# Kernel tuning notes

Hardware: AMD Instinct MI355X
Metric: run time of the kernel (lower is better)

Reference implementation:

```python
import jax, jax.numpy as jnp
import numpy as np

B, S, NQ, H, HD = 2, 4096, 576, 32, 128
HID = H * HD  # 4096


def setup_inputs() -> dict:
    key = jax.random.key(0)
    ks = jax.random.split(key, 7)
    sc = 0.02
    return {
        "hidden_states": jax.random.normal(ks[0], (B, S, HID), jnp.float32),
        "by_pass_hidden_states": jax.random.normal(ks[1], (B, NQ, HID), jnp.float32),
        "attention_mask": jnp.zeros((B, 1, S, NQ), jnp.float32),
        "Wq": jax.random.normal(ks[2], (HID, HID), jnp.float32) * sc,
        "Wk": jax.random.normal(ks[3], (HID, HID), jnp.float32) * sc,
        "Wv": jax.random.normal(ks[4], (HID, HID), jnp.float32) * sc,
        "Wo": jax.random.normal(ks[5], (HID, HID), jnp.float32) * sc,
    }


def reference(hidden_states, by_pass_hidden_states, attention_mask, Wq, Wk, Wv, Wo):
    b, s, _ = hidden_states.shape
    nq = by_pass_hidden_states.shape[1]
    # projections (nn.Linear applies x @ W.T); reshape to (b, heads, len, head_dim)
    q = (hidden_states @ Wq.T).reshape(b, s, H, HD).transpose(0, 2, 1, 3)
    k = (by_pass_hidden_states @ Wk.T).reshape(b, nq, H, HD).transpose(0, 2, 1, 3)
    v = (by_pass_hidden_states @ Wv.T).reshape(b, nq, H, HD).transpose(0, 2, 1, 3)
    # eager QK^T -> mask -> fp32 softmax -> V
    scores = jnp.einsum("bhsd,bhqd->bhsq", q, k) / jnp.sqrt(jnp.float32(HD))
    scores = scores + attention_mask  # (b,1,s,nq) broadcast over heads
    attn = jax.nn.softmax(scores.astype(jnp.float32), axis=-1).astype(q.dtype)
    out = jnp.einsum("bhsq,bhqd->bhsd", attn, v)
    out = out.transpose(0, 2, 1, 3).reshape(b, s, HID)
    return out @ Wo.T
```

## Files before the change

### kernel.cpp

```cpp
#include <hip/hip_runtime.h>
#include <stdint.h>

#define Bn   2
#define Sn   4096
#define NQn  576
#define Hn   32
#define HDn  128
#define HIDn 4096

typedef unsigned short bfu;
typedef short short8 __attribute__((ext_vector_type(8)));
typedef float f32x4 __attribute__((ext_vector_type(4)));

__device__ __forceinline__ bfu f2b(float f) {
  uint32_t x = __builtin_bit_cast(uint32_t, f);
  return (bfu)((x + 0x7fffu + ((x >> 16) & 1u)) >> 16);
}

__device__ __forceinline__ void gload16(const void* g, void* l) {
  __builtin_amdgcn_global_load_lds(
      (const __attribute__((address_space(1))) uint32_t*)g,
      (__attribute__((address_space(3))) uint32_t*)l, 16, 0, 0);
}

__global__ void cast_f32_bf16(const float* __restrict__ in, bfu* __restrict__ out,
                              int n8) {
  int i = blockIdx.x * 256 + threadIdx.x;
  if (i >= n8) return;
  const float4* in4 = (const float4*)in;
  float4 a = in4[2 * i], c = in4[2 * i + 1];
  short8 v;
  v[0] = (short)f2b(a.x); v[1] = (short)f2b(a.y);
  v[2] = (short)f2b(a.z); v[3] = (short)f2b(a.w);
  v[4] = (short)f2b(c.x); v[5] = (short)f2b(c.y);
  v[6] = (short)f2b(c.z); v[7] = (short)f2b(c.w);
  ((short8*)out)[i] = v;
}

template <int WRITE_BF16>
__global__ __launch_bounds__(512, 2)
void gemm_bt256(const bfu* __restrict__ A, const bfu* __restrict__ Bm,
                void* __restrict__ Cout, int M, int N, int K) {
  __shared__ __align__(16) bfu Asm[2][256 * 64];
  __shared__ __align__(16) bfu Bsm[2][256 * 64];
  const int tid = threadIdx.x;
  const int wave = tid >> 6, lane = tid & 63;
  const int lr = lane & 15, kq = lane >> 4;
  const int wm = wave >> 2, wn = wave & 3;
  const long m0 = (long)blockIdx.y * 256, n0 = (long)blockIdx.x * 256;
  const int NT = K >> 6;

  const int c0j = tid >> 3, c0c = tid & 7;
  const int c1j = (512 + tid) >> 3, c1c = tid & 7;
  const bfu* aSrc0 = A + (m0 + c0j) * (long)K + ((c0c ^ (c0j & 7)) * 8);
  const bfu* aSrc1 = A + (m0 + c1j) * (long)K + ((c1c ^ (c1j & 7)) * 8);
  const bfu* bSrc0 = Bm + (n0 + c0j) * (long)K + ((c0c ^ (c0j & 7)) * 8);
  const bfu* bSrc1 = Bm + (n0 + c1j) * (long)K + ((c1c ^ (c1j & 7)) * 8);

  auto stageA = [&](int t, int buf, int half) {
    long koff = (long)t * 64 + (long)half * 128 * K;
    gload16(aSrc0 + koff, &Asm[buf][half * 8192 + (wave * 64) * 8]);
    gload16(aSrc1 + koff, &Asm[buf][half * 8192 + (512 + wave * 64) * 8]);
  };
  auto stageB = [&](int t, int buf, int half) {
    long koff = (long)t * 64 + (long)half * 128 * K;
    gload16(bSrc0 + koff, &Bsm[buf][half * 8192 + (wave * 64) * 8]);
    gload16(bSrc1 + koff, &Bsm[buf][half * 8192 + (512 + wave * 64) * 8]);
  };
  auto ldsA = [&](int buf, int mf, int ks) -> short8 {
    int row = (mf >> 2) * 128 + wm * 64 + (mf & 3) * 16 + lr;
    int off = (row * 128 + ks * 64 + kq * 16) ^ ((row & 7) << 4);
    return *(const short8*)((const char*)Asm[buf] + off);
  };
  auto ldsB = [&](int buf, int nf, int ks) -> short8 {
    int row = (nf >> 1) * 128 + wn * 32 + (nf & 1) * 16 + lr;
    int off = (row * 128 + ks * 64 + kq * 16) ^ ((row & 7) << 4);
    return *(const short8*)((const char*)Bsm[buf] + off);
  };

  f32x4 acc[8][4] = {};

  stageA(0, 0, 0); stageB(0, 0, 0); stageB(0, 0, 1); stageA(0, 0, 1);
  asm volatile("s_waitcnt vmcnt(0)" ::: "memory");
  __builtin_amdgcn_s_barrier();

  for (int t = 0; t < NT; ++t) {
    const int buf = t & 1;
    if (t + 1 < NT) {
      stageA(t + 1, buf ^ 1, 0);
      stageB(t + 1, buf ^ 1, 0);
      stageB(t + 1, buf ^ 1, 1);
      stageA(t + 1, buf ^ 1, 1);
    }
    short8 a0[4][2], a1[4][2], b0[2][2], b1[2][2];
#pragma unroll
    for (int mf = 0; mf < 4; ++mf) {
      a0[mf][0] = ldsA(buf, mf, 0);
      a0[mf][1] = ldsA(buf, mf, 1);
    }
#pragma unroll
    for (int nf = 0; nf < 2; ++nf) {
      b0[nf][0] = ldsB(buf, nf, 0);
      b0[nf][1] = ldsB(buf, nf, 1);
      b1[nf][0] = ldsB(buf, 2 + nf, 0);
      b1[nf][1] = ldsB(buf, 2 + nf, 1);
    }
#pragma unroll
    for (int mf = 0; mf < 4; ++mf)
#pragma unroll
      for (int ks = 0; ks < 2; ++ks)
#pragma unroll
        for (int nf = 0; nf < 2; ++nf)
          acc[mf][nf] = __builtin_amdgcn_mfma_f32_16x16x32_bf16(
              a0[mf][ks], b0[nf][ks], acc[mf][nf], 0, 0, 0);
#pragma unroll
    for (int mf = 0; mf < 4; ++mf) {
      a1[mf][0] = ldsA(buf, 4 + mf, 0);
      a1[mf][1] = ldsA(buf, 4 + mf, 1);
    }
#pragma unroll
    for (int mf = 0; mf < 4; ++mf)
#pragma unroll
      for (int ks = 0; ks < 2; ++ks)
#pragma unroll
        for (int nf = 0; nf < 2; ++nf)
          acc[mf][2 + nf] = __builtin_amdgcn_mfma_f32_16x16x32_bf16(
              a0[mf][ks], b1[nf][ks], acc[mf][2 + nf], 0, 0, 0);
#pragma unroll
    for (int mf = 0; mf < 4; ++mf)
#pragma unroll
      for (int ks = 0; ks < 2; ++ks)
#pragma unroll
        for (int nf = 0; nf < 2; ++nf)
          acc[4 + mf][2 + nf] = __builtin_amdgcn_mfma_f32_16x16x32_bf16(
              a1[mf][ks], b1[nf][ks], acc[4 + mf][2 + nf], 0, 0, 0);
#pragma unroll
    for (int mf = 0; mf < 4; ++mf)
#pragma unroll
      for (int ks = 0; ks < 2; ++ks)
#pragma unroll
        for (int nf = 0; nf < 2; ++nf)
          acc[4 + mf][nf] = __builtin_amdgcn_mfma_f32_16x16x32_bf16(
              a1[mf][ks], b0[nf][ks], acc[4 + mf][nf], 0, 0, 0);
    asm volatile("s_waitcnt vmcnt(0)" ::: "memory");
    __builtin_amdgcn_s_barrier();
  }

#pragma unroll
  for (int mf = 0; mf < 8; ++mf)
#pragma unroll
    for (int nf = 0; nf < 4; ++nf)
#pragma unroll
      for (int r = 0; r < 4; ++r) {
        long row = m0 + (mf >> 2) * 128 + wm * 64 + (mf & 3) * 16 + kq * 4 + r;
        long col = n0 + (nf >> 1) * 128 + wn * 32 + (nf & 1) * 16 + lr;
        float v = acc[mf][nf][r];
        if (WRITE_BF16)
          ((bfu*)Cout)[row * N + col] = f2b(v);
        else
          ((float*)Cout)[row * N + col] = v;
      }
}

template <int WRITE_BF16>
__global__ __launch_bounds__(256, 2)
void gemm_bt(const bfu* __restrict__ A, const bfu* __restrict__ Bm,
             void* __restrict__ Cout, int M, int N, int K) {
  __shared__ __align__(16) bfu As[128 * 32];
  __shared__ __align__(16) bfu Bs[128 * 32];
  const int tid = threadIdx.x;
  const int wave = tid >> 6, lane = tid & 63;
  const int lr = lane & 15, kq = lane >> 4;
  const int wm = wave >> 1, wn = wave & 1;
  const long m0 = (long)blockIdx.y * 128, n0 = (long)blockIdx.x * 128;

  f32x4 acc[4][4] = {};

  for (int kk = 0; kk < K; kk += 32) {
#pragma unroll
    for (int i = 0; i < 2; ++i) {
      int tt = i * 256 + tid;
      long row = tt >> 2;
      int col = (tt & 3) * 8;
      gload16(A + (m0 + row) * K + kk + col, &As[(i * 256 + wave * 64) * 8]);
      gload16(Bm + (n0 + row) * K + kk + col, &Bs[(i * 256 + wave * 64) * 8]);
    }
    __syncthreads();
    short8 a[4], b[4];
#pragma unroll
    for (int mt = 0; mt < 4; ++mt)
      a[mt] = *(const short8*)&As[(wm * 64 + mt * 16 + lr) * 32 + kq * 8];
#pragma unroll
    for (int nt = 0; nt < 4; ++nt)
      b[nt] = *(const short8*)&Bs[(wn * 64 + nt * 16 + lr) * 32 + kq * 8];
#pragma unroll
    for (int mt = 0; mt < 4; ++mt)
#pragma unroll
      for (int nt = 0; nt < 4; ++nt)
        acc[mt][nt] = __builtin_amdgcn_mfma_f32_16x16x32_bf16(
            a[mt], b[nt], acc[mt][nt], 0, 0, 0);
    __syncthreads();
  }
#pragma unroll
  for (int mt = 0; mt < 4; ++mt)
#pragma unroll
    for (int nt = 0; nt < 4; ++nt)
#pragma unroll
      for (int r = 0; r < 4; ++r) {
        long row = m0 + wm * 64 + mt * 16 + kq * 4 + r;
        long col = n0 + wn * 64 + nt * 16 + lr;
        float v = acc[mt][nt][r];
        if (WRITE_BF16)
          ((bfu*)Cout)[row * N + col] = f2b(v);
        else
          ((float*)Cout)[row * N + col] = v;
      }
}

__global__ void transpose_v(const bfu* __restrict__ Vb, bfu* __restrict__ Vt) {
  __shared__ bfu t[32][33];
  const int bh = blockIdx.z;
  const int tq = blockIdx.x;
  const int td = blockIdx.y;
  const int b = bh >> 5, h = bh & 31;
  const int tx = threadIdx.x & 31, ty = threadIdx.x >> 5;
  const bfu* src = Vb + ((long)(b * NQn + tq * 32)) * HIDn + h * HDn + td * 32;
#pragma unroll
  for (int i = 0; i < 32; i += 8) t[ty + i][tx] = src[(long)(ty + i) * HIDn + tx];
  __syncthreads();
  bfu* dst = Vt + ((long)bh * HDn + td * 32) * NQn + tq * 32;
#pragma unroll
  for (int i = 0; i < 32; i += 8) dst[(long)(ty + i) * NQn + tx] = t[tx][ty + i];
}

__global__ __launch_bounds__(512, 2)
void attn_kernel(const bfu* __restrict__ Qb, const bfu* __restrict__ Kb,
                 const bfu* __restrict__ Vt, const float* __restrict__ mask,
                 bfu* __restrict__ AO) {
  __shared__ bfu P[64 * 576];
  __shared__ bfu KV[2][8192];
  __shared__ float red[4][64];
  const int swz = blockIdx.x;
  const int h = swz & (Hn - 1);
  const int b = (swz >> 5) & (Bn - 1);
  const int qt0 = swz >> 6;
  const long q0 = (long)qt0 * 64;
  const int tid = threadIdx.x;
  const int wave = tid >> 6, lane = tid & 63;
  const int lr = lane & 15, kq = lane >> 4;
  const int wk = wave & 3, wq = wave >> 2;
  const float scale = 0.08838834764831845f;

  const bfu* Qbase = Qb + ((long)b * Sn + q0 + wq * 32) * HIDn + h * HDn;
  const bfu* Kblk = Kb + (long)b * NQn * HIDn + h * HDn;
  const bfu* Vblk = Vt + ((long)(b * Hn + h)) * HDn * NQn;
  const float* mbase = mask + ((long)b * Sn + q0 + wq * 32) * NQn + wk * 144;
  char* Pb = (char*)P;

  auto stageK = [&](int mt, int buf) {
#pragma unroll
    for (int i = 0; i < 2; ++i) {
      int c = i * 512 + wave * 64 + lane;
      int j = c >> 4, c16 = c & 15;
      int grow = (j >> 4) * 144 + mt * 16 + (j & 15);
      gload16(Kblk + (long)grow * HIDn + ((c16 ^ (j & 7)) * 8),
              &KV[buf][(i * 512 + wave * 64) * 8]);
    }
  };
  auto stageV = [&](int kt, int buf) {
#pragma unroll
    for (int i = 0; i < 2; ++i) {
      int c = i * 512 + wave * 64 + lane;
      int j = c >> 3, c8 = c & 7;
      gload16(Vblk + (long)j * NQn + kt * 64 + ((c8 ^ (j & 7)) * 8),
              &KV[buf][(i * 512 + wave * 64) * 8]);
    }
  };

  stageK(0, 0);

  short8 qf[2][4];
#pragma unroll
  for (int qt2 = 0; qt2 < 2; ++qt2)
#pragma unroll
    for (int ks = 0; ks < 4; ++ks)
      qf[qt2][ks] =
          *(const short8*)&Qbase[((long)qt2 * 16 + lr) * HIDn + ks * 32 + kq * 8];
  float4 mv[2];
#pragma unroll
  for (int qt2 = 0; qt2 < 2; ++qt2)
    mv[qt2] = *(const float4*)&mbase[((long)qt2 * 16 + lr) * NQn + kq * 4];

  float rsum[2] = {0.f, 0.f};
  for (int mt = 0; mt < 9; ++mt) {
    __syncthreads();
    if (mt < 8) stageK(mt + 1, (mt + 1) & 1);
    const int mtn = (mt < 8) ? mt + 1 : mt;
    float4 mvn[2];
#pragma unroll
    for (int qt2 = 0; qt2 < 2; ++qt2)
      mvn[qt2] =
          *(const float4*)&mbase[((long)qt2 * 16 + lr) * NQn + mtn * 16 + kq * 4];

    const char* kb = (const char*)KV[mt & 1];
#pragma unroll
    for (int qt2 = 0; qt2 < 2; ++qt2) {
      const int row = wq * 32 + qt2 * 16 + lr;
      f32x4 sc = {};
#pragma unroll
      for (int ks = 0; ks < 4; ++ks) {
        short8 kf = *(const short8*)(kb + (((wk * 16 + lr) * 256 + ks * 64 + kq * 16) ^
                                           ((lr & 7) << 4)));
        sc = __builtin_amdgcn_mfma_f32_16x16x32_bf16(kf, qf[qt2][ks], sc, 0, 0, 0);
      }
      float p0 = __expf(sc[0] * scale + mv[qt2].x);
      float p1 = __expf(sc[1] * scale + mv[qt2].y);
      float p2 = __expf(sc[2] * scale + mv[qt2].z);
      float p3 = __expf(sc[3] * scale + mv[qt2].w);
      rsum[qt2] += (p0 + p1) + (p2 + p3);
      uint64_t pk = (uint64_t)f2b(p0) | ((uint64_t)f2b(p1) << 16) |
                    ((uint64_t)f2b(p2) << 32) | ((uint64_t)f2b(p3) << 48);
      int off = (row * 1152 + (wk * 288 + mt * 32 + kq * 8)) ^ ((row & 7) << 4);
      *(uint64_t*)(Pb + off) = pk;
    }
    mv[0] = mvn[0];
    mv[1] = mvn[1];
  }
#pragma unroll
  for (int qt2 = 0; qt2 < 2; ++qt2) {
    rsum[qt2] += __shfl_xor(rsum[qt2], 16, 64);
    rsum[qt2] += __shfl_xor(rsum[qt2], 32, 64);
    if (kq == 0) red[wk][wq * 32 + qt2 * 16 + lr] = rsum[qt2];
  }
  __syncthreads();

  float inv[2];
#pragma unroll
  for (int qt = 0; qt < 2; ++qt) {
    int row = wq * 32 + qt * 16 + lr;
    inv[qt] = 1.0f / ((red[0][row] + red[1][row]) + (red[2][row] + red[3][row]));
  }

  const int wd = wk;
  stageV(0, 0);
  f32x4 o[2][2] = {};
  for (int kt = 0; kt < 9; ++kt) {
    __syncthreads();
    if (kt < 8) stageV(kt + 1, (kt + 1) & 1);
    const char* vb = (const char*)KV[kt & 1];
#pragma unroll
    for (int sub = 0; sub < 2; ++sub) {
      const int ks = kt * 2 + sub;
      short8 vf[2], pf[2];
#pragma unroll
      for (int dt = 0; dt < 2; ++dt)
        vf[dt] = *(const short8*)(vb + (((wd * 32 + dt * 16 + lr) * 128 + sub * 64 +
                                         kq * 16) ^
                                        ((lr & 7) << 4)));
#pragma unroll
      for (int qt = 0; qt < 2; ++qt) {
        int row = wq * 32 + qt * 16 + lr;
        int off = (row * 1152 + (ks * 64 + kq * 16)) ^ ((row & 7) << 4);
        pf[qt] = *(const short8*)(Pb + off);
      }
#pragma unroll
      for (int qt = 0; qt < 2; ++qt)
#pragma unroll
        for (int dt = 0; dt < 2; ++dt)
          o[qt][dt] = __builtin_amdgcn_mfma_f32_16x16x32_bf16(vf[dt], pf[qt],
                                                              o[qt][dt], 0, 0, 0);
    }
  }
#pragma unroll
  for (int qt = 0; qt < 2; ++qt) {
    const long qrow = (long)b * Sn + q0 + wq * 32 + qt * 16 + lr;
    const float iv = inv[qt];
#pragma unroll
    for (int dt = 0; dt < 2; ++dt) {
      uint64_t pk = (uint64_t)f2b(o[qt][dt][0] * iv) |
                    ((uint64_t)f2b(o[qt][dt][1] * iv) << 16) |
                    ((uint64_t)f2b(o[qt][dt][2] * iv) << 32) |
                    ((uint64_t)f2b(o[qt][dt][3] * iv) << 48);
      *(uint64_t*)&AO[qrow * HIDn + h * HDn + wd * 32 + dt * 16 + kq * 4] = pk;
    }
  }
}

extern "C" void kernel_launch(void* const* d_in, const int* in_sizes, int n_in,
                              void* d_out, int out_size, void* d_ws, size_t ws_size,
                              hipStream_t stream) {
  const float* hs = (const float*)d_in[0];
  const float* bp = (const float*)d_in[1];
  const float* mask = (const float*)d_in[2];
  const float* Wq = (const float*)d_in[3];
  const float* Wk = (const float*)d_in[4];
  const float* Wv = (const float*)d_in[5];
  const float* Wo = (const float*)d_in[6];
  float* out = (float*)d_out;

  const long M1 = (long)Bn * Sn;
  const long M2 = (long)Bn * NQn;
  char* ws = (char*)d_ws;
  bfu* hb = (bfu*)(ws + 0);
  bfu* bb = (bfu*)(ws + 67108864);
  bfu* w1 = (bfu*)(ws + 76546048);
  bfu* wkb = (bfu*)(ws + 110100480);
  bfu* wvb = (bfu*)(ws + 143654912);
  bfu* Qb = (bfu*)(ws + 177209344);
  bfu* Kb = (bfu*)(ws + 244318208);
  bfu* Vb = (bfu*)(ws + 253755392);
  bfu* Vt = (bfu*)(ws + 263192576);

  auto cast = [&](const float* src, bfu* dst, long n) {
    int n8 = (int)(n / 8);
    cast_f32_bf16<<<dim3((n8 + 255) / 256), dim3(256), 0, stream>>>(src, dst, n8);
  };
  cast(hs, hb, M1 * HIDn);
  cast(bp, bb, M2 * HIDn);
  cast(Wq, w1, (long)HIDn * HIDn);
  cast(Wk, wkb, (long)HIDn * HIDn);
  cast(Wv, wvb, (long)HIDn * HIDn);

  gemm_bt256<1><<<dim3(HIDn / 256, M1 / 256), dim3(512), 0, stream>>>(
      hb, w1, Qb, (int)M1, HIDn, HIDn);
  gemm_bt<1><<<dim3(HIDn / 128, M2 / 128), dim3(256), 0, stream>>>(
      bb, wkb, Kb, (int)M2, HIDn, HIDn);
  gemm_bt<1><<<dim3(HIDn / 128, M2 / 128), dim3(256), 0, stream>>>(
      bb, wvb, Vb, (int)M2, HIDn, HIDn);

  cast(Wo, w1, (long)HIDn * HIDn);
  transpose_v<<<dim3(NQn / 32, HDn / 32, Bn * Hn), dim3(256), 0, stream>>>(Vb, Vt);

  attn_kernel<<<dim3((Sn / 64) * Bn * Hn), dim3(512), 0, stream>>>(
      Qb, Kb, Vt, mask, hb );

  gemm_bt256<0><<<dim3(HIDn / 256, M1 / 256), dim3(512), 0, stream>>>(
      hb, w1, out, (int)M1, HIDn, HIDn);
}
```

Before: 1.100 ms.

## Fuse attention QK and PV into single pass with register-resident probabilities

Restructures the attention kernel from a two-phase design (store full P row-block in LDS, then a separate PV pass) into a single streaming loop over 32-key tiles. Each wave owns 16 query rows, computes scores, exponentiates, and reshuffles the bf16 probabilities across lanes into an MFMA operand so PV accumulates directly in registers. This drops the large P buffer and the cross-wave sum reduction, cutting LDS use so more blocks can be resident. The trade-off is extra cross-lane shuffles per tile, more accumulator registers, and a V tile layout without an XOR swizzle, which may cause LDS bank conflicts.

```diff
diff --git a/kernel.cpp b/kernel.cpp
--- a/kernel.cpp
+++ b/kernel.cpp
@@ -233,156 +233,122 @@
   for (int i = 0; i < 32; i += 8) dst[(long)(ty + i) * NQn + tx] = t[tx][ty + i];
 }
 
-__global__ __launch_bounds__(512, 2)
+__global__ __launch_bounds__(256, 3)
 void attn_kernel(const bfu* __restrict__ Qb, const bfu* __restrict__ Kb,
                  const bfu* __restrict__ Vt, const float* __restrict__ mask,
                  bfu* __restrict__ AO) {
-  __shared__ bfu P[64 * 576];
-  __shared__ bfu KV[2][8192];
-  __shared__ float red[4][64];
-  const int swz = blockIdx.x;
-  const int h = swz & (Hn - 1);
-  const int b = (swz >> 5) & (Bn - 1);
-  const int qt0 = swz >> 6;
+  __shared__ __align__(16) bfu Ks[2][4096];
+  __shared__ __align__(16) bfu Vs[2][4096];
+  const int bid = blockIdx.x;
+  const int h = bid & (Hn - 1);
+  const int b = (bid >> 5) & (Bn - 1);
+  const int qt0 = bid >> 6;
   const long q0 = (long)qt0 * 64;
   const int tid = threadIdx.x;
   const int wave = tid >> 6, lane = tid & 63;
   const int lr = lane & 15, kq = lane >> 4;
-  const int wk = wave & 3, wq = wave >> 2;
   const float scale = 0.08838834764831845f;
 
-  const bfu* Qbase = Qb + ((long)b * Sn + q0 + wq * 32) * HIDn + h * HDn;
+  const long qrow = (long)b * Sn + q0 + wave * 16 + lr;
   const bfu* Kblk = Kb + (long)b * NQn * HIDn + h * HDn;
   const bfu* Vblk = Vt + ((long)(b * Hn + h)) * HDn * NQn;
-  const float* mbase = mask + ((long)b * Sn + q0 + wq * 32) * NQn + wk * 144;
-  char* Pb = (char*)P;
-
-  auto stageK = [&](int mt, int buf) {
+  const float* mrow = mask + ((long)b * Sn + q0 + wave * 16 + lr) * NQn;
+
+  auto stageK = [&](int kt, int buf) {
 #pragma unroll
     for (int i = 0; i < 2; ++i) {
-      int c = i * 512 + wave * 64 + lane;
+      int c = i * 256 + tid;
       int j = c >> 4, c16 = c & 15;
-      int grow = (j >> 4) * 144 + mt * 16 + (j & 15);
-      gload16(Kblk + (long)grow * HIDn + ((c16 ^ (j & 7)) * 8),
-              &KV[buf][(i * 512 + wave * 64) * 8]);
+      gload16(Kblk + (long)(kt * 32 + j) * HIDn + ((c16 ^ (j & 7)) * 8),
+              &Ks[buf][(i * 256 + wave * 64) * 8]);
     }
   };
   auto stageV = [&](int kt, int buf) {
 #pragma unroll
     for (int i = 0; i < 2; ++i) {
-      int c = i * 512 + wave * 64 + lane;
-      int j = c >> 3, c8 = c & 7;
-      gload16(Vblk + (long)j * NQn + kt * 64 + ((c8 ^ (j & 7)) * 8),
-              &KV[buf][(i * 512 + wave * 64) * 8]);
+      int c = i * 256 + tid;
+      int j = c >> 2, c4 = c & 3;
+      gload16(Vblk + (long)j * NQn + kt * 32 + c4 * 8,
+              &Vs[buf][(i * 256 + wave * 64) * 8]);
     }
   };
 
   stageK(0, 0);
-
-  short8 qf[2][4];
-#pragma unroll
-  for (int qt2 = 0; qt2 < 2; ++qt2)
-#pragma unroll
-    for (int ks = 0; ks < 4; ++ks)
-      qf[qt2][ks] =
-          *(const short8*)&Qbase[((long)qt2 * 16 + lr) * HIDn + ks * 32 + kq * 8];
-  float4 mv[2];
-#pragma unroll
-  for (int qt2 = 0; qt2 < 2; ++qt2)
-    mv[qt2] = *(const float4*)&mbase[((long)qt2 * 16 + lr) * NQn + kq * 4];
-
-  float rsum[2] = {0.f, 0.f};
-  for (int mt = 0; mt < 9; ++mt) {
+  stageV(0, 0);
+
+  const bfu* Qbase = Qb + qrow * HIDn + h * HDn;
+  short8 qf[4];
+#pragma unroll
+  for (int ks = 0; ks < 4; ++ks)
+    qf[ks] = *(const short8*)&Qbase[ks * 32 + kq * 8];
+
+  f32x4 o[8] = {};
+  float rsum = 0.f;
+
+  for (int kt = 0; kt < 18; ++kt) {
     __syncthreads();
-    if (mt < 8) stageK(mt + 1, (mt + 1) & 1);
-    const int mtn = (mt < 8) ? mt + 1 : mt;
-    float4 mvn[2];
-#pragma unroll
-    for (int qt2 = 0; qt2 < 2; ++qt2)
-      mvn[qt2] =
-          *(const float4*)&mbase[((long)qt2 * 16 + lr) * NQn + mtn * 16 + kq * 4];
-
-    const char* kb = (const char*)KV[mt & 1];
-#pragma unroll
-    for (int qt2 = 0; qt2 < 2; ++qt2) {
-      const int row = wq * 32 + qt2 * 16 + lr;
-      f32x4 sc = {};
-#pragma unroll
-      for (int ks = 0; ks < 4; ++ks) {
-        short8 kf = *(const short8*)(kb + (((wk * 16 + lr) * 256 + ks * 64 + kq * 16) ^
-                                           ((lr & 7) << 4)));
-        sc = __builtin_amdgcn_mfma_f32_16x16x32_bf16(kf, qf[qt2][ks], sc, 0, 0, 0);
-      }
-      float p0 = __expf(sc[0] * scale + mv[qt2].x);
-      float p1 = __expf(sc[1] * scale + mv[qt2].y);
-      float p2 = __expf(sc[2] * scale + mv[qt2].z);
-      float p3 = __expf(sc[3] * scale + mv[qt2].w);
-      rsum[qt2] += (p0 + p1) + (p2 + p3);
-      uint64_t pk = (uint64_t)f2b(p0) | ((uint64_t)f2b(p1) << 16) |
-                    ((uint64_t)f2b(p2) << 32) | ((uint64_t)f2b(p3) << 48);
-      int off = (row * 1152 + (wk * 288 + mt * 32 + kq * 8)) ^ ((row & 7) << 4);
-      *(uint64_t*)(Pb + off) = pk;
-    }
-    mv[0] = mvn[0];
-    mv[1] = mvn[1];
+    const int buf = kt & 1;
+    if (kt < 17) {
+      stageK(kt + 1, buf ^ 1);
+      stageV(kt + 1, buf ^ 1);
+    }
+    const char* kb = (const char*)Ks[buf];
+    f32x4 s0 = {}, s1 = {};
+#pragma unroll
+    for (int ks = 0; ks < 4; ++ks) {
+      short8 kf0 = *(const short8*)(kb + ((lr * 256 + ks * 64 + kq * 16) ^
+                                          ((lr & 7) << 4)));
+      short8 kf1 = *(const short8*)(kb + (((16 + lr) * 256 + ks * 64 + kq * 16) ^
+                                          ((lr & 7) << 4)));
+      s0 = __builtin_amdgcn_mfma_f32_16x16x32_bf16(kf0, qf[ks], s0, 0, 0, 0);
+      s1 = __builtin_amdgcn_mfma_f32_16x16x32_bf16(kf1, qf[ks], s1, 0, 0, 0);
+    }
+    float4 m0 = *(const float4*)&mrow[kt * 32 + kq * 4];
+    float4 m1 = *(const float4*)&mrow[kt * 32 + 16 + kq * 4];
+    float p00 = __expf(s0[0] * scale + m0.x), p01 = __expf(s0[1] * scale + m0.y);
+    float p02 = __expf(s0[2] * scale + m0.z), p03 = __expf(s0[3] * scale + m0.w);
+    float p10 = __expf(s1[0] * scale + m1.x), p11 = __expf(s1[1] * scale + m1.y);
+    float p12 = __expf(s1[2] * scale + m1.z), p13 = __expf(s1[3] * scale + m1.w);
+    rsum += ((p00 + p01) + (p02 + p03)) + ((p10 + p11) + (p12 + p13));
+    int pk0_0 = (int)((uint32_t)f2b(p00) | ((uint32_t)f2b(p01) << 16));
+    int pk0_1 = (int)((uint32_t)f2b(p02) | ((uint32_t)f2b(p03) << 16));
+    int pk1_0 = (int)((uint32_t)f2b(p10) | ((uint32_t)f2b(p11) << 16));
+    int pk1_1 = (int)((uint32_t)f2b(p12) | ((uint32_t)f2b(p13) << 16));
+    const int sLo = lr + (((kq & 1) << 1) << 4);
+    const int sHi = sLo + 16;
+    int b0, b1, b2, b3;
+    {
+      int v0 = __shfl(pk0_0, sLo, 64), v1 = __shfl(pk1_0, sLo, 64);
+      b0 = (kq < 2) ? v0 : v1;
+      v0 = __shfl(pk0_1, sLo, 64); v1 = __shfl(pk1_1, sLo, 64);
+      b1 = (kq < 2) ? v0 : v1;
+      v0 = __shfl(pk0_0, sHi, 64); v1 = __shfl(pk1_0, sHi, 64);
+      b2 = (kq < 2) ? v0 : v1;
+      v0 = __shfl(pk0_1, sHi, 64); v1 = __shfl(pk1_1, sHi, 64);
+      b3 = (kq < 2) ? v0 : v1;
+    }
+    int4 pfi = {b0, b1, b2, b3};
+    short8 pfrag = __builtin_bit_cast(short8, pfi);
+    const char* vb = (const char*)Vs[buf];
+#pragma unroll
+    for (int dt = 0; dt < 8; ++dt) {
+      short8 vf = *(const short8*)(vb + ((dt * 16 + lr) * 64 + kq * 16));
+      o[dt] = __builtin_amdgcn_mfma_f32_16x16x32_bf16(vf, pfrag, o[dt], 0, 0, 0);
+    }
   }
-#pragma unroll
-  for (int qt2 = 0; qt2 < 2; ++qt2) {
-    rsum[qt2] += __shfl_xor(rsum[qt2], 16, 64);
-    rsum[qt2] += __shfl_xor(rsum[qt2], 32, 64);
-    if (kq == 0) red[wk][wq * 32 + qt2 * 16 + lr] = rsum[qt2];
-  }
-  __syncthreads();
-
-  float inv[2];
-#pragma unroll
-  for (int qt = 0; qt < 2; ++qt) {
-    int row = wq * 32 + qt * 16 + lr;
-    inv[qt] = 1.0f / ((red[0][row] + red[1][row]) + (red[2][row] + red[3][row]));
-  }
-
-  const int wd = wk;
-  stageV(0, 0);
-  f32x4 o[2][2] = {};
-  for (int kt = 0; kt < 9; ++kt) {
-    __syncthreads();
-    if (kt < 8) stageV(kt + 1, (kt + 1) & 1);
-    const char* vb = (const char*)KV[kt & 1];
-#pragma unroll
-    for (int sub = 0; sub < 2; ++sub) {
-      const int ks = kt * 2 + sub;
-      short8 vf[2], pf[2];
-#pragma unroll
-      for (int dt = 0; dt < 2; ++dt)
-        vf[dt] = *(const short8*)(vb + (((wd * 32 + dt * 16 + lr) * 128 + sub * 64 +
-                                         kq * 16) ^
-                                        ((lr & 7) << 4)));
-#pragma unroll
-      for (int qt = 0; qt < 2; ++qt) {
-        int row = wq * 32 + qt * 16 + lr;
-        int off = (row * 1152 + (ks * 64 + kq * 16)) ^ ((row & 7) << 4);
-        pf[qt] = *(const short8*)(Pb + off);
-      }
-#pragma unroll
-      for (int qt = 0; qt < 2; ++qt)
-#pragma unroll
-        for (int dt = 0; dt < 2; ++dt)
-          o[qt][dt] = __builtin_amdgcn_mfma_f32_16x16x32_bf16(vf[dt], pf[qt],
-                                                              o[qt][dt], 0, 0, 0);
-    }
-  }
-#pragma unroll
-  for (int qt = 0; qt < 2; ++qt) {
-    const long qrow = (long)b * Sn + q0 + wq * 32 + qt * 16 + lr;
-    const float iv = inv[qt];
-#pragma unroll
-    for (int dt = 0; dt < 2; ++dt) {
-      uint64_t pk = (uint64_t)f2b(o[qt][dt][0] * iv) |
-                    ((uint64_t)f2b(o[qt][dt][1] * iv) << 16) |
-                    ((uint64_t)f2b(o[qt][dt][2] * iv) << 32) |
-                    ((uint64_t)f2b(o[qt][dt][3] * iv) << 48);
-      *(uint64_t*)&AO[qrow * HIDn + h * HDn + wd * 32 + dt * 16 + kq * 4] = pk;
-    }
+
+  rsum += __shfl_xor(rsum, 16, 64);
+  rsum += __shfl_xor(rsum, 32, 64);
+  const float inv = 1.0f / rsum;
+
+  bfu* Obase = AO + qrow * HIDn + h * HDn;
+#pragma unroll
+  for (int dt = 0; dt < 8; ++dt) {
+    uint64_t pk = (uint64_t)f2b(o[dt][0] * inv) |
+                  ((uint64_t)f2b(o[dt][1] * inv) << 16) |
+                  ((uint64_t)f2b(o[dt][2] * inv) << 32) |
+                  ((uint64_t)f2b(o[dt][3] * inv) << 48);
+    *(uint64_t*)&Obase[dt * 16 + kq * 4] = pk;
   }
 }
 
@@ -431,7 +397,7 @@
   cast(Wo, w1, (long)HIDn * HIDn);
   transpose_v<<<dim3(NQn / 32, HDn / 32, Bn * Hn), dim3(256), 0, stream>>>(Vb, Vt);
 
-  attn_kernel<<<dim3((Sn / 64) * Bn * Hn), dim3(512), 0, stream>>>(
+  attn_kernel<<<dim3((Sn / 64) * Bn * Hn), dim3(256), 0, stream>>>(
       Qb, Kb, Vt, mask, hb );
 
   gemm_bt256<0><<<dim3(HIDn / 256, M1 / 256), dim3(512), 0, stream>>>(
```

New measurement: 986.3 us. 1.11x faster.
